# Performance work log

Measured on AMD Instinct MI355X. Metric: run time of the kernel, lower is better.

The kernel has to match this reference:

```python
import jax, jax.numpy as jnp
import numpy as np

B, N, C = 8, 2048, 128
K = 16
DILATIONS = (1, 2)
KMAX = K * max(DILATIONS)  # neighbors constructed by DilatedKnnGraph
NEG_SLOPE = 0.2


def setup_inputs() -> dict:
    key = jax.random.key(0)
    ks = jax.random.split(key, 12)
    D = len(DILATIONS)

    def nrm(k, shape, fan_in):
        return jax.random.normal(k, shape, jnp.float32) / np.float32(np.sqrt(fan_in))

    x = jax.random.normal(ks[0], (B, N, C), jnp.float32)
    pos = jax.random.normal(ks[1], (B, N, 3), jnp.float32)
    # PointTransformerConv params per dilation layer (bias-free lin/lin_src/lin_dst, pos_nn=Linear(3,C))
    W_lin = nrm(ks[2], (D, C, C), C)
    W_src = nrm(ks[3], (D, C, C), C)
    W_dst = nrm(ks[4], (D, C, C), C)
    W_pos = nrm(ks[5], (D, 3, C), 3)
    b_pos = jnp.zeros((D, C), jnp.float32)
    # global fusion MLP: Linear(C+3, C) + LeakyReLU(0.2)
    Wg = nrm(ks[6], (C + 3, C), C + 3)
    bg = jnp.zeros((C,), jnp.float32)
    # final MLP: Linear(C,C) + LeakyReLU(0.2) + Linear(C,3)
    W1 = nrm(ks[7], (C, C), C)
    b1 = jnp.zeros((C,), jnp.float32)
    W2 = nrm(ks[8], (C, 3), C)
    b2 = jnp.zeros((3,), jnp.float32)
    return dict(x=x, pos=pos, W_lin=W_lin, W_src=W_src, W_dst=W_dst,
                W_pos=W_pos, b_pos=b_pos, Wg=Wg, bg=bg, W1=W1, b1=b1, W2=W2, b2=b2)


def _knn(p):
    # p: [N, 3] -> [N, KMAX] neighbor indices sorted by ascending distance (self excluded)
    sq = jnp.sum(p * p, axis=-1)
    d2 = sq[:, None] + sq[None, :] - 2.0 * (p @ p.T)
    d2 = d2 + jnp.eye(p.shape[0], dtype=p.dtype) * jnp.float32(1e10)
    _, idx = jax.lax.top_k(-d2, KMAX)
    return idx


def reference(x, pos, W_lin, W_src, W_dst, W_pos, b_pos, Wg, bg, W1, b1, W2, b2):
    nbr = jax.vmap(_knn)(pos)  # [B, N, KMAX]
    self_idx = jnp.broadcast_to(jnp.arange(N)[None, :, None], (B, N, 1))
    gather = jax.vmap(lambda arr, idx: arr[idx])  # per-cloud fancy gather

    h = None
    for li, d in enumerate(DILATIONS):
        # Dilated neighbor selection: every d-th of sorted neighbors, keep K, plus self loop
        idx = jnp.concatenate([nbr[:, :, ::d][:, :, :K], self_idx], axis=-1)  # [B, N, K+1]
        pos_j = gather(pos, idx)  # [B, N, K+1, 3]
        # delta_ij = pos_nn(pos_i - pos_j)
        delta = jnp.einsum('bnkt,tc->bnkc', pos[:, :, None, :] - pos_j, W_pos[li]) + b_pos[li]
        s = x @ W_src[li]   # lin_src
        v = x @ W_lin[li]   # value projection
        t = x @ W_dst[li]   # lin_dst
        # alpha_ij = lin_dst(x_i) - lin_src(x_j) + delta ; per-channel softmax over neighbors
        alpha = t[:, :, None, :] - gather(s, idx) + delta  # [B, N, K+1, C]
        w = jax.nn.softmax(alpha, axis=2)
        h_ = jnp.sum(w * (gather(v, idx) + delta), axis=2)  # [B, N, C]
        h = h_ if h is None else h + h_

    h2 = jax.nn.leaky_relu(jnp.concatenate([x, pos], axis=-1) @ Wg + bg, NEG_SLOPE)
    h = h + h2
    res = jax.nn.leaky_relu(h @ W1 + b1, NEG_SLOPE) @ W2 + b2
    return res + pos  # add_points=True
```

## Files before the change

### kernel.cpp

```cpp
#include <hip/hip_runtime.h>

#define BB 8
#define NN 2048
#define CC 128
#define KMAX 32
#define NEG 0.2f
#define CH 8
#define CHSZ (NN / CH)
#define CAP 32

using bf16x8 = __attribute__((ext_vector_type(8))) short;
using f32x4  = __attribute__((ext_vector_type(4))) float;

__device__ __forceinline__ unsigned int f2key(float f) {
  unsigned int b = __float_as_uint(f);
  return (b & 0x80000000u) ? ~b : (b | 0x80000000u);
}

__device__ __forceinline__ float sq3(float x, float y, float z) {
  return __fadd_rn(__fadd_rn(__fmul_rn(x, x), __fmul_rn(y, y)), __fmul_rn(z, z));
}

__device__ __forceinline__ float d2np(float px, float py, float pz, float sqq,
                                      float qx, float qy, float qz, float sqj) {
  float dot = __fmaf_rn(pz, qz, __fmaf_rn(py, qy, __fmul_rn(px, qx)));
  return __fsub_rn(__fadd_rn(sqq, sqj), __fmul_rn(2.0f, dot));
}

__device__ __forceinline__ unsigned short f2bf(float f) {
  unsigned int u = __float_as_uint(f);
  return (unsigned short)((u + 0x7fffu + ((u >> 16) & 1u)) >> 16);
}
__device__ __forceinline__ float bf2f(unsigned short u) {
  return __uint_as_float(((unsigned int)u) << 16);
}

__device__ __forceinline__ bf16x8 cvt8(const float* __restrict__ p) {
  float4 a = *(const float4*)(p);
  float4 b = *(const float4*)(p + 4);
  bf16x8 r;
  r[0] = (short)f2bf(a.x); r[1] = (short)f2bf(a.y);
  r[2] = (short)f2bf(a.z); r[3] = (short)f2bf(a.w);
  r[4] = (short)f2bf(b.x); r[5] = (short)f2bf(b.y);
  r[6] = (short)f2bf(b.z); r[7] = (short)f2bf(b.w);
  return r;
}

__device__ __forceinline__ int paddr(int c, int jj) { return (c << 8) + (jj ^ c); }

__device__ __forceinline__ void knn_body(int bx, int tid,
                                         const float* __restrict__ pos,
                                         int* __restrict__ nbr,
                                         float4* __restrict__ sp4,
                                         unsigned char* __restrict__ sbuf) {
  int b = bx >> 6;
  int qbase = (bx & 63) * 32;
  const float* pb = pos + (size_t)b * NN * 3;
  for (int t = tid; t < NN; t += 256) {
    float xx = pb[t * 3 + 0];
    float yy = pb[t * 3 + 1];
    float zz = pb[t * 3 + 2];
    sp4[paddr(t >> 8, t & 255)] = make_float4(xx, yy, zz, sq3(xx, yy, zz));
  }
  __syncthreads();

  int q = qbase + (tid >> 3);
  int c = tid & 7;
  float4 pq = sp4[paddr(q >> 8, q & 255)];
  float px = pq.x, py = pq.y, pz = pq.z;
  float sqq = pq.w;
  int j0 = c * CHSZ;

  const float SENT = 3.0e38f;
  float a0 = SENT, a1 = SENT, a2 = SENT, a3 = SENT;
#pragma unroll 4
  for (int jj = 0; jj < CHSZ; ++jj) {
    float4 pj = sp4[paddr(c, jj)];
    float d2 = d2np(px, py, pz, sqq, pj.x, pj.y, pj.z, pj.w);
    if (j0 + jj == q) d2 = SENT;
    float m0 = fmaxf(a0, d2); a0 = fminf(a0, d2);
    float m1 = fmaxf(a1, m0); a1 = fminf(a1, m0);
    float m2 = fmaxf(a2, m1); a2 = fminf(a2, m1);
    a3 = fminf(a3, m2);
  }

  float T = a3;
  T = fmaxf(T, __shfl_xor(T, 1));
  T = fmaxf(T, __shfl_xor(T, 2));
  T = fmaxf(T, __shfl_xor(T, 4));

  unsigned int ak[KMAX];
  int ai[KMAX];
#pragma unroll
  for (int k = 0; k < KMAX; ++k) { ak[k] = 0xFFFFFFFFu; ai[k] = 0xFFFF; }

  int sbase = tid * CAP;
  auto drain = [&](int cnt2) {
    for (int u = 0; u < cnt2; ++u) {
      int jj2 = (int)sbuf[sbase + u];
      int j = j0 + jj2;
      float4 pj = sp4[paddr(c, jj2)];
      float d2 = d2np(px, py, pz, sqq, pj.x, pj.y, pj.z, pj.w);
      unsigned int key = f2key(d2);
      if (key < ak[KMAX - 1]) {
#pragma unroll
        for (int k = KMAX - 1; k >= 1; --k) {
          bool ck  = key < ak[k];
          bool ckm = key < ak[k - 1];
          unsigned int tk = ckm ? ak[k - 1] : key;
          int          ti = ckm ? ai[k - 1] : j;
          ak[k] = ck ? tk : ak[k];
          ai[k] = ck ? ti : ai[k];
        }
        bool c0b = key < ak[0];
        ak[0] = c0b ? key : ak[0];
        ai[0] = c0b ? j : ai[0];
      }
    }
  };

  int cnt = 0;
  for (int jj = 0; jj < CHSZ; ++jj) {
    float4 pj = sp4[paddr(c, jj)];
    float d2 = d2np(px, py, pz, sqq, pj.x, pj.y, pj.z, pj.w);
    bool pass = (d2 <= T) && (j0 + jj != q);
    if (pass) {
      if (cnt == CAP) { drain(CAP); cnt = 0; }
      sbuf[sbase + cnt] = (unsigned char)jj;
      ++cnt;
    }
  }
  drain(cnt);

  __syncthreads();
  unsigned int* mkey = (unsigned int*)sp4;
  unsigned char* mjj = sbuf;
#pragma unroll
  for (int k = 0; k < KMAX; ++k) {
    mkey[k * 256 + tid] = ak[k];
    mjj[k * 256 + tid] = (unsigned char)(ai[k] & 255);
  }
  __syncthreads();

  int hd = 0;
  unsigned long long packed =
      ((unsigned long long)ak[0] << 11) | (unsigned int)((c << 8) | (ai[0] & 255));
  int* onb = nbr + ((size_t)(b * NN + q)) * KMAX;
#pragma unroll
  for (int r = 0; r < KMAX; ++r) {
    unsigned long long m = packed;
    unsigned long long s1 = __shfl_xor(m, 1); m = m < s1 ? m : s1;
    unsigned long long s2 = __shfl_xor(m, 2); m = m < s2 ? m : s2;
    unsigned long long s4 = __shfl_xor(m, 4); m = m < s4 ? m : s4;
    if (c == 0) onb[r] = (int)(m & 0x7FF);
    if (packed == m) {
      ++hd;
      if (hd < KMAX) {
        unsigned int kv = mkey[hd * 256 + tid];
        unsigned int jv = mjj[hd * 256 + tid];
        packed = ((unsigned long long)kv << 11) | (unsigned int)((c << 8) | jv);
      } else {
        packed = ~0ull;
      }
    }
  }
}

__device__ __forceinline__ void proj_body(int z, int mx, int tid,
                                          const float* __restrict__ x,
                                          const unsigned short* __restrict__ wf,
                                          unsigned short* __restrict__ pb16) {
  const size_t MCSZ = (size_t)BB * NN * CC;
  size_t base;
  int mul;
  if (z < 4) {
    base = (size_t)(z & 1) * 2 * MCSZ + (size_t)(z >> 1);
    mul = 2;
  } else {
    base = (size_t)z * MCSZ;
    mul = 1;
  }
  int wave = tid >> 6;
  int lane = tid & 63;
  int m0 = (mx * 4 + wave) * 16;
  int quad = lane >> 4;
  int am = m0 + (lane & 15);

  f32x4 acc[8];
#pragma unroll
  for (int nt = 0; nt < 8; ++nt) acc[nt] = (f32x4){0.f, 0.f, 0.f, 0.f};

  const unsigned short* wz = wf + (size_t)z * (8 * 4 * 64 * 8);
#pragma unroll
  for (int ks = 0; ks < 4; ++ks) {
    bf16x8 a = cvt8(x + (size_t)am * CC + ks * 32 + quad * 8);
#pragma unroll
    for (int nt = 0; nt < 8; ++nt) {
      bf16x8 bfr = *(const bf16x8*)(wz + (size_t)(((nt * 4 + ks) * 64 + lane) * 8));
      acc[nt] = __builtin_amdgcn_mfma_f32_16x16x32_bf16(a, bfr, acc[nt], 0, 0, 0);
    }
  }

  int col0 = lane & 15;
#pragma unroll
  for (int nt = 0; nt < 8; ++nt)
#pragma unroll
    for (int r = 0; r < 4; ++r) {
      size_t idx = (size_t)(m0 + quad * 4 + r) * CC + nt * 16 + col0;
      pb16[base + idx * mul] = f2bf(acc[nt][r]);
    }
}

__device__ __forceinline__ void wg_body(int mx, int tid,
                                        const float* __restrict__ x,
                                        const float* __restrict__ pos,
                                        const unsigned short* __restrict__ wf,
                                        const float* __restrict__ wgtail,
                                        const float* __restrict__ bg,
                                        float* __restrict__ h) {
  int wave = tid >> 6;
  int lane = tid & 63;
  int m0 = (mx * 4 + wave) * 16;
  int quad = lane >> 4;
  int am = m0 + (lane & 15);

  f32x4 acc[8];
#pragma unroll
  for (int nt = 0; nt < 8; ++nt) acc[nt] = (f32x4){0.f, 0.f, 0.f, 0.f};

  const unsigned short* wz = wf + (size_t)6 * (8 * 4 * 64 * 8);
#pragma unroll
  for (int ks = 0; ks < 4; ++ks) {
    bf16x8 a = cvt8(x + (size_t)am * CC + ks * 32 + quad * 8);
#pragma unroll
    for (int nt = 0; nt < 8; ++nt) {
      bf16x8 b = *(const bf16x8*)(wz + (size_t)(((nt * 4 + ks) * 64 + lane) * 8));
      acc[nt] = __builtin_amdgcn_mfma_f32_16x16x32_bf16(a, b, acc[nt], 0, 0, 0);
    }
  }

  float posr[4][3];
#pragma unroll
  for (int r = 0; r < 4; ++r) {
    int m = m0 + quad * 4 + r;
    posr[r][0] = pos[m * 3 + 0];
    posr[r][1] = pos[m * 3 + 1];
    posr[r][2] = pos[m * 3 + 2];
  }

  int col0 = lane & 15;
#pragma unroll
  for (int nt = 0; nt < 8; ++nt) {
    int col = nt * 16 + col0;
    float bv = bg[col];
    float t0 = wgtail[col];
    float t1 = wgtail[CC + col];
    float t2 = wgtail[2 * CC + col];
#pragma unroll
    for (int r = 0; r < 4; ++r) {
      float v = acc[nt][r] + bv
              + posr[r][0] * t0 + posr[r][1] * t1 + posr[r][2] * t2;
      v = v > 0.f ? v : NEG * v;
      h[(size_t)(m0 + quad * 4 + r) * CC + col] = v;
    }
  }
}

__global__ __launch_bounds__(256) void fused_front(
    const float* __restrict__ pos,
    int* __restrict__ nbr,
    const float* __restrict__ x,
    const unsigned short* __restrict__ wf,
    unsigned short* __restrict__ pb16,
    const float* __restrict__ wgtail,
    const float* __restrict__ bg,
    float* __restrict__ h) {
  __shared__ float4 sp4[CH * 256];
  __shared__ unsigned char sbuf[256 * CAP];

  if (blockIdx.x < 512) {
    knn_body(blockIdx.x, threadIdx.x, pos, nbr, sp4, sbuf);
  } else if (blockIdx.x < 2048) {
    int bx = blockIdx.x - 512;
    proj_body(bx >> 8, bx & 255, threadIdx.x, x, wf, pb16);
  } else {
    wg_body(blockIdx.x - 2048, threadIdx.x, x, pos, wf, wgtail, bg, h);
  }
}

__global__ __launch_bounds__(256) void knn_p1(const float* __restrict__ pos,
                                              int* __restrict__ nbr) {
  __shared__ float4 sp4[CH * 256];
  __shared__ unsigned char sbuf[256 * CAP];
  knn_body(blockIdx.x, threadIdx.x, pos, nbr, sp4, sbuf);
}

__global__ __launch_bounds__(256) void wcvt(const float* __restrict__ Wa,
                                            const float* __restrict__ Wb,
                                            const float* __restrict__ Wc,
                                            const float* __restrict__ Wgm,
                                            const float* __restrict__ W1m,
                                            unsigned short* __restrict__ wf,
                                            const float* __restrict__ Wpos,
                                            const float* __restrict__ pos,
                                            float* __restrict__ pp) {
  if (blockIdx.x < 64) {
    int t = blockIdx.x * 256 + threadIdx.x;
    int lane = t & 63;
    int ks = (t >> 6) & 3;
    int nt = (t >> 8) & 7;
    int z = t >> 11;
    const float* W = (z < 2) ? (Wa + (size_t)z * CC * CC)
                   : (z < 4) ? (Wb + (size_t)(z - 2) * CC * CC)
                   : (z < 6) ? (Wc + (size_t)(z - 4) * CC * CC)
                   : (z == 6) ? Wgm : W1m;
    int n = nt * 16 + (lane & 15);
    int kb = ks * 32 + (lane >> 4) * 8;
    unsigned short* o = wf + (size_t)t * 8;
#pragma unroll
    for (int j = 0; j < 8; ++j)
      o[j] = f2bf(W[(size_t)(kb + j) * CC + n]);
  } else {
    int pb2 = blockIdx.x - 64;
    int l = threadIdx.x >> 7;
    int c = threadIdx.x & 127;
    const float* Wp = Wpos + (size_t)l * 3 * CC;
    float w0 = Wp[c], w1 = Wp[CC + c], w2 = Wp[2 * CC + c];
    float* ppl = pp + (size_t)l * ((size_t)BB * NN * CC);
    int m0 = pb2 * 128;
    for (int mi = 0; mi < 128; ++mi) {
      int m = m0 + mi;
      float xx = pos[m * 3 + 0];
      float yy = pos[m * 3 + 1];
      float zz = pos[m * 3 + 2];
      ppl[(size_t)m * CC + c] = __fmaf_rn(zz, w2, __fmaf_rn(yy, w1, __fmul_rn(xx, w0)));
    }
  }
}

__global__ __launch_bounds__(256) void proj_fly(const float* __restrict__ x,
                                                const unsigned short* __restrict__ wf,
                                                unsigned short* __restrict__ pb16) {
  proj_body(blockIdx.z, blockIdx.x, threadIdx.x, x, wf, pb16);
}
__global__ __launch_bounds__(256) void wg_fly(const float* __restrict__ x,
                                              const float* __restrict__ pos,
                                              const unsigned short* __restrict__ wf,
                                              const float* __restrict__ wgtail,
                                              const float* __restrict__ bg,
                                              float* __restrict__ h) {
  wg_body(blockIdx.x, threadIdx.x, x, pos, wf, wgtail, bg, h);
}

__global__ __launch_bounds__(128) void attn2_kernel(
    const int* __restrict__ nbr,
    const unsigned int* __restrict__ sv0, const unsigned int* __restrict__ sv1,
    const unsigned short* __restrict__ t0, const unsigned short* __restrict__ t1,
    const float* __restrict__ pp, const float* __restrict__ bpos,
    const float* __restrict__ h, unsigned short* __restrict__ hb) {
  int b = blockIdx.x & 7;
  int n = blockIdx.x >> 3;
  int bn = (b << 11) + n;
  int c = threadIdx.x;

  const int* nb = nbr + (size_t)bn * KMAX;
  int idxs[KMAX];
#pragma unroll
  for (int u = 0; u < KMAX / 4; ++u) {
    int4 v4 = *(const int4*)(nb + u * 4);
    idxs[u * 4 + 0] = v4.x; idxs[u * 4 + 1] = v4.y;
    idxs[u * 4 + 2] = v4.z; idxs[u * 4 + 3] = v4.w;
  }

  float ht = h[(size_t)bn * CC + c];

#pragma unroll
  for (int l = 0; l < 2; ++l) {
    int dil = l + 1;
    const unsigned int* sv = l ? sv1 : sv0;
    const unsigned short* t = l ? t1 : t0;
    const float* ppl = pp + (size_t)l * ((size_t)BB * NN * CC);
    float bp = bpos[(size_t)l * CC + c];
    float tc = bf2f(t[(size_t)bn * CC + c]);
    float ppi = ppl[(size_t)bn * CC + c];

    int id[17];
#pragma unroll
    for (int j = 0; j < 17; ++j) id[j] = (j < 16) ? idxs[j * dil] : n;

    unsigned int svw[17];
    float pj[17];
#pragma unroll
    for (int j = 0; j < 17; ++j)
      svw[j] = sv[((size_t)(b * NN + id[j])) * CC + c];
#pragma unroll
    for (int j = 0; j < 17; ++j)
      pj[j] = ppl[((size_t)(b * NN + id[j])) * CC + c];

    float alpha[17], del[17];
#pragma unroll
    for (int j = 0; j < 17; ++j) {
      float d = ppi - pj[j] + bp;
      del[j] = d;
      float sc = bf2f((unsigned short)(svw[j] & 0xFFFFu));
      alpha[j] = tc - sc + d;
    }
    float m8[8];
#pragma unroll
    for (int j = 0; j < 8; ++j) m8[j] = fmaxf(alpha[j], alpha[j + 8]);
    float m4a = fmaxf(m8[0], m8[1]), m4b = fmaxf(m8[2], m8[3]);
    float m4c = fmaxf(m8[4], m8[5]), m4d = fmaxf(m8[6], m8[7]);
    float mx = fmaxf(fmaxf(fmaxf(m4a, m4b), fmaxf(m4c, m4d)), alpha[16]);

    float sum = 0.f;
#pragma unroll
    for (int j = 0; j < 17; ++j) {
      float w = __expf(alpha[j] - mx);
      alpha[j] = w;
      sum += w;
    }
    float inv = 1.f / sum;

    float hc = 0.f;
#pragma unroll
    for (int j = 0; j < 17; ++j) {
      float vc = bf2f((unsigned short)(svw[j] >> 16));
      hc += alpha[j] * (vc + del[j]);
    }
    ht += hc * inv;
  }

  hb[(size_t)bn * CC + c] = f2bf(ht);
}

__global__ __launch_bounds__(256) void mfma_w1_final(
    const unsigned short* __restrict__ hb,
    const unsigned short* __restrict__ wz,
    const float* __restrict__ b1,
    const float* __restrict__ W2,
    const float* __restrict__ b2,
    const float* __restrict__ pos,
    float* __restrict__ out) {
  int wave = threadIdx.x >> 6;
  int lane = threadIdx.x & 63;
  int m0 = (blockIdx.x * 4 + wave) * 16;
  int quad = lane >> 4;
  int am = m0 + (lane & 15);

  f32x4 acc[8];
#pragma unroll
  for (int nt = 0; nt < 8; ++nt) acc[nt] = (f32x4){0.f, 0.f, 0.f, 0.f};

#pragma unroll
  for (int ks = 0; ks < 4; ++ks) {
    bf16x8 a = *(const bf16x8*)(hb + (size_t)am * CC + ks * 32 + quad * 8);
#pragma unroll
    for (int nt = 0; nt < 8; ++nt) {
      bf16x8 b = *(const bf16x8*)(wz + (size_t)(((nt * 4 + ks) * 64 + lane) * 8));
      acc[nt] = __builtin_amdgcn_mfma_f32_16x16x32_bf16(a, b, acc[nt], 0, 0, 0);
    }
  }

  int col0 = lane & 15;
  float part[4][3];
#pragma unroll
  for (int r = 0; r < 4; ++r)
#pragma unroll
    for (int d = 0; d < 3; ++d) part[r][d] = 0.f;

#pragma unroll
  for (int nt = 0; nt < 8; ++nt) {
    int col = nt * 16 + col0;
    float bv = b1[col];
    float w20 = W2[col * 3 + 0];
    float w21 = W2[col * 3 + 1];
    float w22 = W2[col * 3 + 2];
#pragma unroll
    for (int r = 0; r < 4; ++r) {
      float gv = acc[nt][r] + bv;
      gv = gv > 0.f ? gv : NEG * gv;
      part[r][0] = fmaf(gv, w20, part[r][0]);
      part[r][1] = fmaf(gv, w21, part[r][1]);
      part[r][2] = fmaf(gv, w22, part[r][2]);
    }
  }

#pragma unroll
  for (int off = 8; off >= 1; off >>= 1) {
#pragma unroll
    for (int r = 0; r < 4; ++r)
#pragma unroll
      for (int d = 0; d < 3; ++d)
        part[r][d] += __shfl_xor(part[r][d], off);
  }

  if (col0 == 0) {
#pragma unroll
    for (int r = 0; r < 4; ++r) {
      int m = m0 + quad * 4 + r;
#pragma unroll
      for (int d = 0; d < 3; ++d)
        out[(size_t)m * 3 + d] = part[r][d] + b2[d] + pos[(size_t)m * 3 + d];
    }
  }
}

extern "C" void kernel_launch(void* const* d_in, const int* in_sizes, int n_in,
                              void* d_out, int out_size, void* d_ws, size_t ws_size,
                              hipStream_t stream) {
  const float* x     = (const float*)d_in[0];
  const float* pos   = (const float*)d_in[1];
  const float* W_lin = (const float*)d_in[2];
  const float* W_src = (const float*)d_in[3];
  const float* W_dst = (const float*)d_in[4];
  const float* W_pos = (const float*)d_in[5];
  const float* b_pos = (const float*)d_in[6];
  const float* Wg    = (const float*)d_in[7];
  const float* bg    = (const float*)d_in[8];
  const float* W1    = (const float*)d_in[9];
  const float* b1    = (const float*)d_in[10];
  const float* W2    = (const float*)d_in[11];
  const float* b2    = (const float*)d_in[12];
  float* out = (float*)d_out;

  const size_t M = (size_t)BB * NN;
  const size_t MC = M * CC;

  char* ws = (char*)d_ws;
  int* nbr = (int*)ws;
  unsigned short* cand = (unsigned short*)(ws + M * KMAX * sizeof(int));
  float* fb = (float*)(ws + M * KMAX * sizeof(int) + M * CH * KMAX * sizeof(unsigned short));
  unsigned short* pb16 = (unsigned short*)fb;
  unsigned int* sv0 = (unsigned int*)pb16;
  unsigned int* sv1 = sv0 + MC;
  unsigned short* tb0 = pb16 + 4 * MC;
  unsigned short* tb1 = pb16 + 5 * MC;
  float* h = fb + 5 * MC;
  float* pp = fb + 6 * MC;

  const size_t BASE = M * KMAX * sizeof(int) + M * CH * KMAX * sizeof(unsigned short)
                    + 8 * MC * sizeof(float);
  const size_t XB_BYTES = MC * sizeof(unsigned short);
  const size_t WF_BYTES = 8 * 16384 * sizeof(unsigned short);
  const size_t FRAG = (size_t)(8 * 4 * 64 * 8);
  bool fused_ok = ws_size >= BASE + XB_BYTES + WF_BYTES;

  if (fused_ok) {
    unsigned short* hb = (unsigned short*)(ws + BASE);
    unsigned short* wf = (unsigned short*)(ws + BASE + XB_BYTES);

    wcvt<<<192, 256, 0, stream>>>(W_src, W_lin, W_dst, Wg, W1, wf, W_pos, pos, pp);
    fused_front<<<2304, 256, 0, stream>>>(pos, nbr, x, wf, pb16,
                                          Wg + 128 * CC, bg, h);
    attn2_kernel<<<M, 128, 0, stream>>>(nbr, sv0, sv1, tb0, tb1,
                                        pp, b_pos, h, hb);
    mfma_w1_final<<<M / 64, 256, 0, stream>>>(hb, wf + 7 * FRAG, b1,
                                              W2, b2, pos, out);
  } else {
    unsigned short* hb = cand;
    unsigned short* wf = cand + MC;
    knn_p1<<<512, 256, 0, stream>>>(pos, nbr);
    wcvt<<<192, 256, 0, stream>>>(W_src, W_lin, W_dst, Wg, W1, wf, W_pos, pos, pp);
    proj_fly<<<dim3(256, 1, 6), 256, 0, stream>>>(x, wf, pb16);
    wg_fly<<<256, 256, 0, stream>>>(x, pos, wf, Wg + 128 * CC, bg, h);
    attn2_kernel<<<M, 128, 0, stream>>>(nbr, sv0, sv1, tb0, tb1,
                                        pp, b_pos, h, hb);
    mfma_w1_final<<<M / 64, 256, 0, stream>>>(hb, wf + 7 * FRAG, b1,
                                              W2, b2, pos, out);
  }
}
```

Before: 193.3 us.

## Split KNN candidate scan across 16 lanes per query instead of 8

```diff
diff --git a/kernel.cpp b/kernel.cpp
--- a/kernel.cpp
+++ b/kernel.cpp
@@ -6,7 +6,8 @@
 #define KMAX 32
 #define NEG 0.2f
 #define CH 8
-#define CHSZ (NN / CH)
+#define NSUB 16
+#define SUBSZ (NN / NSUB)
 #define CAP 32
 
 using bf16x8 = __attribute__((ext_vector_type(8))) short;
@@ -46,38 +47,40 @@
   return r;
 }
 
-__device__ __forceinline__ int paddr(int c, int jj) { return (c << 8) + (jj ^ c); }
+__device__ __forceinline__ int paddr16(int l, int jj) { return (l << 7) + (jj ^ (l & 7)); }
 
 __device__ __forceinline__ void knn_body(int bx, int tid,
                                          const float* __restrict__ pos,
                                          int* __restrict__ nbr,
                                          float4* __restrict__ sp4,
                                          unsigned char* __restrict__ sbuf) {
-  int b = bx >> 6;
-  int qbase = (bx & 63) * 32;
+  int b = bx >> 7;
+  int qbase = (bx & 127) * 16;
   const float* pb = pos + (size_t)b * NN * 3;
   for (int t = tid; t < NN; t += 256) {
     float xx = pb[t * 3 + 0];
     float yy = pb[t * 3 + 1];
     float zz = pb[t * 3 + 2];
-    sp4[paddr(t >> 8, t & 255)] = make_float4(xx, yy, zz, sq3(xx, yy, zz));
+    sp4[paddr16(t >> 7, t & 127)] = make_float4(xx, yy, zz, sq3(xx, yy, zz));
   }
   __syncthreads();
 
-  int q = qbase + (tid >> 3);
-  int c = tid & 7;
-  float4 pq = sp4[paddr(q >> 8, q & 255)];
+  int q = qbase + (tid >> 4);
+  int l = tid & 15;
+  float4 pq = sp4[paddr16(q >> 7, q & 127)];
   float px = pq.x, py = pq.y, pz = pq.z;
   float sqq = pq.w;
-  int j0 = c * CHSZ;
+  int j0 = l * SUBSZ;
 
   const float SENT = 3.0e38f;
+  int selfjj = ((q >> 7) == l) ? (q & 127) : 1024;
+
   float a0 = SENT, a1 = SENT, a2 = SENT, a3 = SENT;
 #pragma unroll 4
-  for (int jj = 0; jj < CHSZ; ++jj) {
-    float4 pj = sp4[paddr(c, jj)];
+  for (int jj = 0; jj < SUBSZ; ++jj) {
+    float4 pj = sp4[paddr16(l, jj)];
     float d2 = d2np(px, py, pz, sqq, pj.x, pj.y, pj.z, pj.w);
-    if (j0 + jj == q) d2 = SENT;
+    if (jj == selfjj) d2 = SENT;
     float m0 = fmaxf(a0, d2); a0 = fminf(a0, d2);
     float m1 = fmaxf(a1, m0); a1 = fminf(a1, m0);
     float m2 = fmaxf(a2, m1); a2 = fminf(a2, m1);
@@ -88,6 +91,7 @@
   T = fmaxf(T, __shfl_xor(T, 1));
   T = fmaxf(T, __shfl_xor(T, 2));
   T = fmaxf(T, __shfl_xor(T, 4));
+  T = fmaxf(T, __shfl_xor(T, 8));
 
   unsigned int ak[KMAX];
   int ai[KMAX];
@@ -99,7 +103,7 @@
     for (int u = 0; u < cnt2; ++u) {
       int jj2 = (int)sbuf[sbase + u];
       int j = j0 + jj2;
-      float4 pj = sp4[paddr(c, jj2)];
+      float4 pj = sp4[paddr16(l, jj2)];
       float d2 = d2np(px, py, pz, sqq, pj.x, pj.y, pj.z, pj.w);
       unsigned int key = f2key(d2);
       if (key < ak[KMAX - 1]) {
@@ -120,10 +124,10 @@
   };
 
   int cnt = 0;
-  for (int jj = 0; jj < CHSZ; ++jj) {
-    float4 pj = sp4[paddr(c, jj)];
+  for (int jj = 0; jj < SUBSZ; ++jj) {
+    float4 pj = sp4[paddr16(l, jj)];
     float d2 = d2np(px, py, pz, sqq, pj.x, pj.y, pj.z, pj.w);
-    bool pass = (d2 <= T) && (j0 + jj != q);
+    bool pass = (d2 <= T) && (jj != selfjj);
     if (pass) {
       if (cnt == CAP) { drain(CAP); cnt = 0; }
       sbuf[sbase + cnt] = (unsigned char)jj;
@@ -138,13 +142,13 @@
 #pragma unroll
   for (int k = 0; k < KMAX; ++k) {
     mkey[k * 256 + tid] = ak[k];
-    mjj[k * 256 + tid] = (unsigned char)(ai[k] & 255);
+    mjj[k * 256 + tid] = (unsigned char)(ai[k] & 127);
   }
   __syncthreads();
 
   int hd = 0;
   unsigned long long packed =
-      ((unsigned long long)ak[0] << 11) | (unsigned int)((c << 8) | (ai[0] & 255));
+      ((unsigned long long)ak[0] << 11) | (unsigned int)(ai[0] & 0x7FF);
   int* onb = nbr + ((size_t)(b * NN + q)) * KMAX;
 #pragma unroll
   for (int r = 0; r < KMAX; ++r) {
@@ -152,13 +156,14 @@
     unsigned long long s1 = __shfl_xor(m, 1); m = m < s1 ? m : s1;
     unsigned long long s2 = __shfl_xor(m, 2); m = m < s2 ? m : s2;
     unsigned long long s4 = __shfl_xor(m, 4); m = m < s4 ? m : s4;
-    if (c == 0) onb[r] = (int)(m & 0x7FF);
+    unsigned long long s8 = __shfl_xor(m, 8); m = m < s8 ? m : s8;
+    if (l == 0) onb[r] = (int)(m & 0x7FF);
     if (packed == m) {
       ++hd;
       if (hd < KMAX) {
         unsigned int kv = mkey[hd * 256 + tid];
         unsigned int jv = mjj[hd * 256 + tid];
-        packed = ((unsigned long long)kv << 11) | (unsigned int)((c << 8) | jv);
+        packed = ((unsigned long long)kv << 11) | (unsigned int)((l << 7) | jv);
       } else {
         packed = ~0ull;
       }
@@ -275,22 +280,22 @@
     const float* __restrict__ wgtail,
     const float* __restrict__ bg,
     float* __restrict__ h) {
-  __shared__ float4 sp4[CH * 256];
+  __shared__ float4 sp4[NSUB * SUBSZ];
   __shared__ unsigned char sbuf[256 * CAP];
 
-  if (blockIdx.x < 512) {
+  if (blockIdx.x < 1024) {
     knn_body(blockIdx.x, threadIdx.x, pos, nbr, sp4, sbuf);
-  } else if (blockIdx.x < 2048) {
-    int bx = blockIdx.x - 512;
+  } else if (blockIdx.x < 2560) {
+    int bx = blockIdx.x - 1024;
     proj_body(bx >> 8, bx & 255, threadIdx.x, x, wf, pb16);
   } else {
-    wg_body(blockIdx.x - 2048, threadIdx.x, x, pos, wf, wgtail, bg, h);
+    wg_body(blockIdx.x - 2560, threadIdx.x, x, pos, wf, wgtail, bg, h);
   }
 }
 
 __global__ __launch_bounds__(256) void knn_p1(const float* __restrict__ pos,
                                               int* __restrict__ nbr) {
-  __shared__ float4 sp4[CH * 256];
+  __shared__ float4 sp4[NSUB * SUBSZ];
   __shared__ unsigned char sbuf[256 * CAP];
   knn_body(blockIdx.x, threadIdx.x, pos, nbr, sp4, sbuf);
 }
@@ -550,7 +555,7 @@
     unsigned short* wf = (unsigned short*)(ws + BASE + XB_BYTES);
 
     wcvt<<<192, 256, 0, stream>>>(W_src, W_lin, W_dst, Wg, W1, wf, W_pos, pos, pp);
-    fused_front<<<2304, 256, 0, stream>>>(pos, nbr, x, wf, pb16,
+    fused_front<<<2816, 256, 0, stream>>>(pos, nbr, x, wf, pb16,
                                           Wg + 128 * CC, bg, h);
     attn2_kernel<<<M, 128, 0, stream>>>(nbr, sv0, sv1, tb0, tb1,
                                         pp, b_pos, h, hb);
@@ -559,7 +564,7 @@
   } else {
     unsigned short* hb = cand;
     unsigned short* wf = cand + MC;
-    knn_p1<<<512, 256, 0, stream>>>(pos, nbr);
+    knn_p1<<<1024, 256, 0, stream>>>(pos, nbr);
     wcvt<<<192, 256, 0, stream>>>(W_src, W_lin, W_dst, Wg, W1, wf, W_pos, pos, pp);
     proj_fly<<<dim3(256, 1, 6), 256, 0, stream>>>(x, wf, pb16);
     wg_fly<<<256, 256, 0, stream>>>(x, pos, wf, Wg + 128 * CC, bg, h);
```

New measurement: 209.7 us. 1.08x slower.
